# Kernel tuning notes

Hardware: AMD Instinct MI355X
Metric: run time of the kernel (lower is better)

## Reference

```python
import jax, jax.numpy as jnp
import numpy as np

N, NODE_DIM, EDGE_DIM, HID, NREL = 1024, 128, 32, 128, 16


def _sage(h, adj, W, b):
    # agg = mean over (weighted) neighbors: (adj @ h) / (deg + 1e-6)
    agg = (adj @ h) / (jnp.sum(adj, axis=1, keepdims=True) + 1e-6)
    return jax.nn.relu(jnp.concatenate([h, agg], axis=1) @ W.T + b)


def setup_inputs() -> dict:
    key = jax.random.key(0)
    ks = jax.random.split(key, 12)
    s1 = 1.0 / np.sqrt(2 * NODE_DIM)
    s2 = 1.0 / np.sqrt(2 * HID)
    s3 = 1.0 / np.sqrt(2 * HID + EDGE_DIM)
    s4 = 1.0 / np.sqrt(HID)
    return {
        "node_feat": jax.random.normal(ks[0], (N, NODE_DIM), jnp.float32),
        "edge_feat": jax.random.normal(ks[1], (N, N, EDGE_DIM), jnp.float32),
        "adj": jax.random.uniform(ks[2], (N, N), jnp.float32),
        "W_g1": jax.random.normal(ks[3], (HID, 2 * NODE_DIM), jnp.float32) * s1,
        "b_g1": jax.random.normal(ks[4], (HID,), jnp.float32) * s1,
        "W_g2": jax.random.normal(ks[5], (HID, 2 * HID), jnp.float32) * s2,
        "b_g2": jax.random.normal(ks[6], (HID,), jnp.float32) * s2,
        "W_c1": jax.random.normal(ks[7], (HID, 2 * HID + EDGE_DIM), jnp.float32) * s3,
        "b_c1": jax.random.normal(ks[8], (HID,), jnp.float32) * s3,
        "W_c2": jax.random.normal(ks[9], (NREL, HID), jnp.float32) * s4,
        "b_c2": jax.random.normal(ks[10], (NREL,), jnp.float32) * s4,
    }


def reference(node_feat, edge_feat, adj, W_g1, b_g1, W_g2, b_g2, W_c1, b_c1, W_c2, b_c2):
    h = _sage(node_feat, adj, W_g1, b_g1)          # [N, HID]
    h = _sage(h, adj, W_g2, b_g2)                  # [N, HID]
    H = h.shape[1]
    # Split first classifier layer over [h_i ; h_j ; e_ij] to avoid a huge concat.
    Wa, Wb, We = W_c1[:, :H], W_c1[:, H:2 * H], W_c1[:, 2 * H:]
    pre = ((h @ Wa.T)[:, None, :]
           + (h @ Wb.T)[None, :, :]
           + jnp.einsum('ije,he->ijh', edge_feat, We)
           + b_c1)                                  # [N, N, HID]
    logits = jax.nn.relu(pre) @ W_c2.T + b_c2       # [N, N, NREL]
    # diagonal (i == j) stays zero, matching the skipped loop iterations
    n = logits.shape[0]
    mask = 1.0 - jnp.eye(n, dtype=logits.dtype)
    return logits * mask[:, :, None]
```

## Files before the change

kernel.cpp:

```cpp
#include <hip/hip_runtime.h>
#include <hip/hip_bf16.h>
#include <stdint.h>

constexpr int NN = 1024;
constexpr int DD = 128;
constexpr int EDIM = 32;
constexpr int NR = 16;

using short4v = __attribute__((ext_vector_type(4))) short;
using short8v = __attribute__((ext_vector_type(8))) short;
using f32x4   = __attribute__((ext_vector_type(4))) float;

__device__ __forceinline__ short f2bf(float x) {
  __hip_bfloat16 h = __float2bfloat16(x);
  return __builtin_bit_cast(short, h);
}

__device__ __forceinline__ void nt_store4(float* p, const float4& v) {
  f32x4 t;
  t[0] = v.x; t[1] = v.y; t[2] = v.z; t[3] = v.w;
  __builtin_nontemporal_store(t, (f32x4*)p);
}

__global__ __launch_bounds__(256) void k_transp(const float* __restrict__ src,
                                                short* __restrict__ dst) {
  __shared__ float tile[32][33];
  int b = blockIdx.x;
  int r0 = (b & 31) * 32, c0 = (b >> 5) * 32;
  int t = threadIdx.x;
  {
    int rr = t >> 3, c4 = (t & 7) * 4;
    float4 v = *(const float4*)(src + (size_t)(r0 + rr) * DD + c0 + c4);
    tile[rr][c4]     = v.x;
    tile[rr][c4 + 1] = v.y;
    tile[rr][c4 + 2] = v.z;
    tile[rr][c4 + 3] = v.w;
  }
  __syncthreads();
  {
    int cc = t >> 3, r4 = (t & 7) * 4;
    short4v s;
    s[0] = f2bf(tile[r4 + 0][cc]);
    s[1] = f2bf(tile[r4 + 1][cc]);
    s[2] = f2bf(tile[r4 + 2][cc]);
    s[3] = f2bf(tile[r4 + 3][cc]);
    *(short4v*)(dst + (size_t)(c0 + cc) * NN + r0 + r4) = s;
  }
}

__global__ __launch_bounds__(256) void k_adjmm(const short* __restrict__ XT,
                                               const float* __restrict__ adj,
                                               float* __restrict__ part) {
  int t = threadIdx.x;
  int w = t >> 6, lane = t & 63;
  int c = lane & 15, g = lane >> 4;
  int b = blockIdx.x;
  int ic = b & 15, hc = (b >> 4) & 3, kc = b >> 6;
  int i0 = ic * 64 + w * 16, h0 = hc * 32;
  size_t kb = (size_t)kc * 256 + 8 * g;

  f32x4 acc0 = {0, 0, 0, 0}, acc1 = {0, 0, 0, 0};
  const short* xa0 = XT + (size_t)(h0 + c) * NN + kb;
  const short* xa1 = XT + (size_t)(h0 + 16 + c) * NN + kb;
  const float* ba  = adj + (size_t)(i0 + c) * NN + kb;
  #pragma unroll
  for (int ks = 0; ks < 8; ++ks) {
    short8v a0 = *(const short8v*)(xa0 + ks * 32);
    short8v a1 = *(const short8v*)(xa1 + ks * 32);
    float4 b0 = *(const float4*)(ba + ks * 32);
    float4 b1 = *(const float4*)(ba + ks * 32 + 4);
    short8v bb;
    bb[0] = f2bf(b0.x); bb[1] = f2bf(b0.y); bb[2] = f2bf(b0.z); bb[3] = f2bf(b0.w);
    bb[4] = f2bf(b1.x); bb[5] = f2bf(b1.y); bb[6] = f2bf(b1.z); bb[7] = f2bf(b1.w);
    acc0 = __builtin_amdgcn_mfma_f32_16x16x32_bf16(a0, bb, acc0, 0, 0, 0);
    acc1 = __builtin_amdgcn_mfma_f32_16x16x32_bf16(a1, bb, acc1, 0, 0, 0);
  }
  float* p0 = part + ((size_t)kc * NN + (i0 + c)) * DD + h0 + 4 * g;
  float4 o0 = {acc0[0], acc0[1], acc0[2], acc0[3]};
  float4 o1 = {acc1[0], acc1[1], acc1[2], acc1[3]};
  *(float4*)(p0)      = o0;
  *(float4*)(p0 + 16) = o1;
}

__global__ __launch_bounds__(256) void k_dense1(const float* __restrict__ X,
                                                const float* __restrict__ part,
                                                const float* __restrict__ adj,
                                                const float* __restrict__ W,
                                                const float* __restrict__ b,
                                                float* __restrict__ out,
                                                float* __restrict__ rsinv) {
  __shared__ float sagg[2][128];
  __shared__ float red[4];
  int t = threadIdx.x;
  int ig = t >> 7, h = t & 127;
  int i = blockIdx.x * 2 + ig;
  {
    const float4* ar = (const float4*)(adj + (size_t)i * NN);
    float4 v0 = ar[h * 2], v1 = ar[h * 2 + 1];
    float s = v0.x + v0.y + v0.z + v0.w + v1.x + v1.y + v1.z + v1.w;
    #pragma unroll
    for (int off = 32; off > 0; off >>= 1) s += __shfl_down(s, off, 64);
    if ((t & 63) == 0) red[t >> 6] = s;
  }
  __syncthreads();
  float rs = 1.0f / (red[ig * 2] + red[ig * 2 + 1] + 1e-6f);
  if (h == 0) rsinv[i] = rs;
  {
    float ss = 0.f;
    #pragma unroll
    for (int kc = 0; kc < 4; ++kc) ss += part[(size_t)kc * NN * DD + (size_t)i * DD + h];
    sagg[ig][h] = ss * rs;
  }
  __syncthreads();
  const float4* xr = (const float4*)(X + (size_t)i * DD);
  const float4* ar = (const float4*)(&sagg[ig][0]);
  const float4* w1 = (const float4*)(W + (size_t)h * 256);
  const float4* w2 = (const float4*)(W + (size_t)h * 256 + DD);
  float acc = b[h];
  #pragma unroll 8
  for (int k = 0; k < 32; ++k) {
    float4 x = xr[k], w = w1[k];
    acc += x.x * w.x + x.y * w.y + x.z * w.z + x.w * w.w;
  }
  #pragma unroll 8
  for (int k = 0; k < 32; ++k) {
    float4 y = ar[k], w = w2[k];
    acc += y.x * w.x + y.y * w.y + y.z * w.z + y.w * w.w;
  }
  out[(size_t)i * DD + h] = fmaxf(acc, 0.f);
}

__global__ __launch_bounds__(256) void k_dense2ab(const float* __restrict__ X,
                                                  const float* __restrict__ part,
                                                  const float* __restrict__ rsinv,
                                                  const float* __restrict__ W,
                                                  const float* __restrict__ b,
                                                  const float* __restrict__ Wc1,
                                                  const float* __restrict__ bc1,
                                                  float* __restrict__ Aib,
                                                  float* __restrict__ Bmat) {
  __shared__ float sagg[2][128];
  __shared__ float sh2[2][128];
  int t = threadIdx.x;
  int ig = t >> 7, h = t & 127;
  int i = blockIdx.x * 2 + ig;
  {
    float ss = 0.f;
    #pragma unroll
    for (int kc = 0; kc < 4; ++kc) ss += part[(size_t)kc * NN * DD + (size_t)i * DD + h];
    sagg[ig][h] = ss * rsinv[i];
  }
  __syncthreads();
  {
    const float4* xr = (const float4*)(X + (size_t)i * DD);
    const float4* ar = (const float4*)(&sagg[ig][0]);
    const float4* w1 = (const float4*)(W + (size_t)h * 256);
    const float4* w2 = (const float4*)(W + (size_t)h * 256 + DD);
    float acc = b[h];
    #pragma unroll 8
    for (int k = 0; k < 32; ++k) {
      float4 x = xr[k], w = w1[k];
      acc += x.x * w.x + x.y * w.y + x.z * w.z + x.w * w.w;
    }
    #pragma unroll 8
    for (int k = 0; k < 32; ++k) {
      float4 y = ar[k], w = w2[k];
      acc += y.x * w.x + y.y * w.y + y.z * w.z + y.w * w.w;
    }
    sh2[ig][h] = fmaxf(acc, 0.f);
  }
  __syncthreads();
  const float4* xr = (const float4*)(&sh2[ig][0]);
  const float4* wa = (const float4*)(Wc1 + (size_t)h * 288);
  const float4* wb = (const float4*)(Wc1 + (size_t)h * 288 + 128);
  float aa = bc1[h], bb = 0.f;
  #pragma unroll 8
  for (int k = 0; k < 32; ++k) {
    float4 x = xr[k];
    float4 a = wa[k], b2 = wb[k];
    aa += x.x * a.x + x.y * a.y + x.z * a.z + x.w * a.w;
    bb += x.x * b2.x + x.y * b2.y + x.z * b2.z + x.w * b2.w;
  }
  Aib[(size_t)i * DD + h] = aa;
  Bmat[(size_t)i * DD + h] = bb;
}

#define EDGE_BODY(T, S, PF) do {                                              \
    float4 a_ = eA##S, b_ = eB##S;                                            \
    if (PF) {                                                                 \
      const float* p_ = ebl + (size_t)((T) + 6) * ((size_t)NN * EDIM);        \
      eA##S = *(const float4*)p_;                                             \
      eB##S = *(const float4*)(p_ + 4);                                       \
    }                                                                         \
    short8v ef_;                                                              \
    ef_[0]=f2bf(a_.x); ef_[1]=f2bf(a_.y); ef_[2]=f2bf(a_.z); ef_[3]=f2bf(a_.w); \
    ef_[4]=f2bf(b_.x); ef_[5]=f2bf(b_.y); ef_[6]=f2bf(b_.z); ef_[7]=f2bf(b_.w); \
    char* pw_ = psm + (((T) & 1) << 12);                                      \
    const float* ap_ = aibs + (T) * 128 + 4 * g;                              \
    _Pragma("unroll")                                                         \
    for (int n = 0; n < 8; ++n) {                                             \
      float4 av_ = *(const float4*)(ap_ + 16 * n);                            \
      f32x4 ci_;                                                              \
      ci_[0] = av_.x + bjv[n].x; ci_[1] = av_.y + bjv[n].y;                   \
      ci_[2] = av_.z + bjv[n].z; ci_[3] = av_.w + bjv[n].w;                   \
      f32x4 acc_ = __builtin_amdgcn_mfma_f32_16x16x32_bf16(weF[n], ef_, ci_, 0, 0, 0); \
      short4v pk_;                                                            \
      pk_[0] = f2bf(fmaxf(acc_[0], 0.f)); pk_[1] = f2bf(fmaxf(acc_[1], 0.f)); \
      pk_[2] = f2bf(fmaxf(acc_[2], 0.f)); pk_[3] = f2bf(fmaxf(acc_[3], 0.f)); \
      *(short4v*)(pw_ + (((n >> 1) << 10) + ((n & 1) << 9) + wroff)) = pk_;   \
    }                                                                         \
  } while (0)

#define G2(G2T, OREG) do {                                                    \
    f32x4 a2_;                                                                \
    a2_[0] = bc2v.x; a2_[1] = bc2v.y; a2_[2] = bc2v.z; a2_[3] = bc2v.w;       \
    const char* pp_ = psm + (((G2T) & 1) << 12);                              \
    _Pragma("unroll")                                                         \
    for (int kk = 0; kk < 4; ++kk) {                                          \
      short8v pb_ = *(const short8v*)(pp_ + ((kk << 10) + rdP));              \
      a2_ = __builtin_amdgcn_mfma_f32_16x16x32_bf16(wcF[kk], pb_, a2_, 0, 0, 0); \
    }                                                                         \
    bool dg_ = (j == i0 + (G2T));                                             \
    OREG.x = dg_ ? 0.f : a2_[0];                                              \
    OREG.y = dg_ ? 0.f : a2_[1];                                              \
    OREG.z = dg_ ? 0.f : a2_[2];                                              \
    OREG.w = dg_ ? 0.f : a2_[3];                                              \
  } while (0)

#define FLUSH(BASE) do {                                                      \
    nt_store4(out + ((size_t)(i0 + (BASE) + 0) * NN + j) * NR + 4 * g, o0);   \
    nt_store4(out + ((size_t)(i0 + (BASE) + 1) * NN + j) * NR + 4 * g, o1);   \
    nt_store4(out + ((size_t)(i0 + (BASE) + 2) * NN + j) * NR + 4 * g, o2);   \
    nt_store4(out + ((size_t)(i0 + (BASE) + 3) * NN + j) * NR + 4 * g, o3);   \
  } while (0)

__global__ __launch_bounds__(256, 1) void k_edge(const float* __restrict__ edge,
                                                 const float* __restrict__ Wc1,
                                                 const float* __restrict__ Wc2,
                                                 const float* __restrict__ bc2,
                                                 const float* __restrict__ Aib,
                                                 const float* __restrict__ Bmat,
                                                 float* __restrict__ out) {
  __shared__ __align__(16) char psm_all[4][2][4096];
  __shared__ __align__(16) float aibs[16 * 128];
  int tid = threadIdx.x;
  int w = tid >> 6, lane = tid & 63;
  int c = lane & 15, g = lane >> 4;
  int ig = blockIdx.x >> 4, jg = blockIdx.x & 15;
  int i0 = ig * 16;
  int j0w = jg * 64 + w * 16;
  int j = j0w + c;

  {
    int ii = tid >> 4, h8 = (tid & 15) * 8;
    const float4* s = (const float4*)(Aib + (size_t)(i0 + ii) * DD + h8);
    *(float4*)(aibs + ii * 128 + h8)     = s[0];
    *(float4*)(aibs + ii * 128 + h8 + 4) = s[1];
  }

  short8v weF[8];
  #pragma unroll
  for (int n = 0; n < 8; ++n) {
    const float* p = Wc1 + (size_t)(16 * n + c) * 288 + 256 + 8 * g;
    float4 f0 = *(const float4*)p;
    float4 f1 = *(const float4*)(p + 4);
    short8v s;
    s[0]=f2bf(f0.x); s[1]=f2bf(f0.y); s[2]=f2bf(f0.z); s[3]=f2bf(f0.w);
    s[4]=f2bf(f1.x); s[5]=f2bf(f1.y); s[6]=f2bf(f1.z); s[7]=f2bf(f1.w);
    weF[n] = s;
  }
  short8v wcF[4];
  #pragma unroll
  for (int kk = 0; kk < 4; ++kk) {
    const float* p = Wc2 + (size_t)c * DD + 32 * kk + 8 * g;
    float4 f0 = *(const float4*)p;
    float4 f1 = *(const float4*)(p + 4);
    short8v s;
    s[0]=f2bf(f0.x); s[1]=f2bf(f0.y); s[2]=f2bf(f0.z); s[3]=f2bf(f0.w);
    s[4]=f2bf(f1.x); s[5]=f2bf(f1.y); s[6]=f2bf(f1.z); s[7]=f2bf(f1.w);
    wcF[kk] = s;
  }
  float4 bc2v = *(const float4*)(bc2 + 4 * g);
  float4 bjv[8];
  #pragma unroll
  for (int n = 0; n < 8; ++n)
    bjv[n] = *(const float4*)(Bmat + (size_t)j * DD + 16 * n + 4 * g);

  __syncthreads();

  char* psm = &psm_all[w][0][0];
  const float* ebl = edge + ((size_t)i0 * NN + j) * EDIM + 8 * g;
  int wroff = (c << 4) + ((g & 1) << 3) + ((g >> 1) << 8);
  int rdP   = (g << 8) + (c << 4);

  float4 o0, o1, o2, o3;

  float4 eA0, eB0, eA1, eB1, eA2, eB2, eA3, eB3, eA4, eB4, eA5, eB5;
  {
    const size_t STP = (size_t)NN * EDIM;
    eA0 = *(const float4*)(ebl);            eB0 = *(const float4*)(ebl + 4);
    eA1 = *(const float4*)(ebl + STP);      eB1 = *(const float4*)(ebl + STP + 4);
    eA2 = *(const float4*)(ebl + 2 * STP);  eB2 = *(const float4*)(ebl + 2 * STP + 4);
    eA3 = *(const float4*)(ebl + 3 * STP);  eB3 = *(const float4*)(ebl + 3 * STP + 4);
    eA4 = *(const float4*)(ebl + 4 * STP);  eB4 = *(const float4*)(ebl + 4 * STP + 4);
    eA5 = *(const float4*)(ebl + 5 * STP);  eB5 = *(const float4*)(ebl + 5 * STP + 4);
  }

  EDGE_BODY(0, 0, 1);
  EDGE_BODY(1, 1, 1);  G2(0, o0);
  EDGE_BODY(2, 2, 1);  G2(1, o1);
  EDGE_BODY(3, 3, 1);  G2(2, o2);
  EDGE_BODY(4, 4, 1);  G2(3, o3);  FLUSH(0);
  EDGE_BODY(5, 5, 1);  G2(4, o0);
  EDGE_BODY(6, 0, 1);  G2(5, o1);
  EDGE_BODY(7, 1, 1);  G2(6, o2);
  EDGE_BODY(8, 2, 1);  G2(7, o3);  FLUSH(4);
  EDGE_BODY(9, 3, 1);  G2(8, o0);
  EDGE_BODY(10, 4, 0); G2(9, o1);
  EDGE_BODY(11, 5, 0); G2(10, o2);
  EDGE_BODY(12, 0, 0); G2(11, o3); FLUSH(8);
  EDGE_BODY(13, 1, 0); G2(12, o0);
  EDGE_BODY(14, 2, 0); G2(13, o1);
  EDGE_BODY(15, 3, 0); G2(14, o2);
  G2(15, o3); FLUSH(12);
}

extern "C" void kernel_launch(void* const* d_in, const int* in_sizes, int n_in,
                              void* d_out, int out_size, void* d_ws, size_t ws_size,
                              hipStream_t stream) {
  const float* node_feat = (const float*)d_in[0];
  const float* edge_feat = (const float*)d_in[1];
  const float* adj  = (const float*)d_in[2];
  const float* W_g1 = (const float*)d_in[3];
  const float* b_g1 = (const float*)d_in[4];
  const float* W_g2 = (const float*)d_in[5];
  const float* b_g2 = (const float*)d_in[6];
  const float* W_c1 = (const float*)d_in[7];
  const float* b_c1 = (const float*)d_in[8];
  const float* W_c2 = (const float*)d_in[9];
  const float* b_c2 = (const float*)d_in[10];
  float* out = (float*)d_out;

  float* ws    = (float*)d_ws;
  float* rsinv = ws;
  float* part  = ws + 1024;
  float* h1    = part + 4 * NN * DD;
  float* Aib   = h1 + NN * DD;
  float* Bmat  = Aib + NN * DD;
  short* XT1   = (short*)(Bmat + NN * DD);
  short* XT2   = XT1 + DD * NN;

  k_transp<<<128, 256, 0, stream>>>(node_feat, XT1);
  k_adjmm<<<256, 256, 0, stream>>>(XT1, adj, part);
  k_dense1<<<512, 256, 0, stream>>>(node_feat, part, adj, W_g1, b_g1, h1, rsinv);
  k_transp<<<128, 256, 0, stream>>>(h1, XT2);
  k_adjmm<<<256, 256, 0, stream>>>(XT2, adj, part);
  k_dense2ab<<<512, 256, 0, stream>>>(h1, part, rsinv, W_g2, b_g2, W_c1, b_c1, Aib, Bmat);
  k_edge<<<1024, 256, 0, stream>>>(edge_feat, W_c1, W_c2, b_c2, Aib, Bmat, out);
}
```

Before: 122.8 us.

## Fuse transpose into adj matmul and cut edge-kernel registers for higher occupancy

```diff
diff --git a/kernel.cpp b/kernel.cpp
--- a/kernel.cpp
+++ b/kernel.cpp
@@ -16,53 +16,44 @@
   return __builtin_bit_cast(short, h);
 }
 
-__device__ __forceinline__ void nt_store4(float* p, const float4& v) {
-  f32x4 t;
-  t[0] = v.x; t[1] = v.y; t[2] = v.z; t[3] = v.w;
-  __builtin_nontemporal_store(t, (f32x4*)p);
-}
-
-__global__ __launch_bounds__(256) void k_transp(const float* __restrict__ src,
-                                                short* __restrict__ dst) {
-  __shared__ float tile[32][33];
-  int b = blockIdx.x;
-  int r0 = (b & 31) * 32, c0 = (b >> 5) * 32;
-  int t = threadIdx.x;
-  {
-    int rr = t >> 3, c4 = (t & 7) * 4;
-    float4 v = *(const float4*)(src + (size_t)(r0 + rr) * DD + c0 + c4);
-    tile[rr][c4]     = v.x;
-    tile[rr][c4 + 1] = v.y;
-    tile[rr][c4 + 2] = v.z;
-    tile[rr][c4 + 3] = v.w;
-  }
-  __syncthreads();
-  {
-    int cc = t >> 3, r4 = (t & 7) * 4;
-    short4v s;
-    s[0] = f2bf(tile[r4 + 0][cc]);
-    s[1] = f2bf(tile[r4 + 1][cc]);
-    s[2] = f2bf(tile[r4 + 2][cc]);
-    s[3] = f2bf(tile[r4 + 3][cc]);
-    *(short4v*)(dst + (size_t)(c0 + cc) * NN + r0 + r4) = s;
-  }
-}
-
-__global__ __launch_bounds__(256) void k_adjmm(const short* __restrict__ XT,
+__device__ __forceinline__ void nt_store4(float* p, const f32x4& v) {
+  __builtin_nontemporal_store(v, (f32x4*)p);
+}
+
+__global__ __launch_bounds__(256) void k_adjmm(const float* __restrict__ X,
                                                const float* __restrict__ adj,
                                                float* __restrict__ part) {
+  __shared__ short xt[32][264];
   int t = threadIdx.x;
   int w = t >> 6, lane = t & 63;
   int c = lane & 15, g = lane >> 4;
   int b = blockIdx.x;
   int ic = b & 15, hc = (b >> 4) & 3, kc = b >> 6;
   int i0 = ic * 64 + w * 16, h0 = hc * 32;
-  size_t kb = (size_t)kc * 256 + 8 * g;
+  int k0 = kc * 256;
+
+  {
+    const float* xr = X + (size_t)(k0 + t) * DD + h0;
+    #pragma unroll
+    for (int c8 = 0; c8 < 4; ++c8) {
+      float4 v0 = *(const float4*)(xr + c8 * 8);
+      float4 v1 = *(const float4*)(xr + c8 * 8 + 4);
+      xt[c8 * 8 + 0][t] = f2bf(v0.x);
+      xt[c8 * 8 + 1][t] = f2bf(v0.y);
+      xt[c8 * 8 + 2][t] = f2bf(v0.z);
+      xt[c8 * 8 + 3][t] = f2bf(v0.w);
+      xt[c8 * 8 + 4][t] = f2bf(v1.x);
+      xt[c8 * 8 + 5][t] = f2bf(v1.y);
+      xt[c8 * 8 + 6][t] = f2bf(v1.z);
+      xt[c8 * 8 + 7][t] = f2bf(v1.w);
+    }
+  }
+  __syncthreads();
 
   f32x4 acc0 = {0, 0, 0, 0}, acc1 = {0, 0, 0, 0};
-  const short* xa0 = XT + (size_t)(h0 + c) * NN + kb;
-  const short* xa1 = XT + (size_t)(h0 + 16 + c) * NN + kb;
-  const float* ba  = adj + (size_t)(i0 + c) * NN + kb;
+  const short* xa0 = &xt[c][8 * g];
+  const short* xa1 = &xt[16 + c][8 * g];
+  const float* ba  = adj + (size_t)(i0 + c) * NN + k0 + 8 * g;
   #pragma unroll
   for (int ks = 0; ks < 8; ++ks) {
     short8v a0 = *(const short8v*)(xa0 + ks * 32);
@@ -185,10 +176,11 @@
   Bmat[(size_t)i * DD + h] = bb;
 }
 
+
 #define EDGE_BODY(T, S, PF) do {                                              \
     float4 a_ = eA##S, b_ = eB##S;                                            \
     if (PF) {                                                                 \
-      const float* p_ = ebl + (size_t)((T) + 6) * ((size_t)NN * EDIM);        \
+      const float* p_ = ebl + (size_t)((T) + 4) * ((size_t)NN * EDIM);        \
       eA##S = *(const float4*)p_;                                             \
       eB##S = *(const float4*)(p_ + 4);                                       \
     }                                                                         \
@@ -200,9 +192,10 @@
     _Pragma("unroll")                                                         \
     for (int n = 0; n < 8; ++n) {                                             \
       float4 av_ = *(const float4*)(ap_ + 16 * n);                            \
+      float4 bv_ = *(const float4*)(bp + 16 * n);           \
       f32x4 ci_;                                                              \
-      ci_[0] = av_.x + bjv[n].x; ci_[1] = av_.y + bjv[n].y;                   \
-      ci_[2] = av_.z + bjv[n].z; ci_[3] = av_.w + bjv[n].w;                   \
+      ci_[0] = av_.x + bv_.x; ci_[1] = av_.y + bv_.y;                         \
+      ci_[2] = av_.z + bv_.z; ci_[3] = av_.w + bv_.w;                         \
       f32x4 acc_ = __builtin_amdgcn_mfma_f32_16x16x32_bf16(weF[n], ef_, ci_, 0, 0, 0); \
       short4v pk_;                                                            \
       pk_[0] = f2bf(fmaxf(acc_[0], 0.f)); pk_[1] = f2bf(fmaxf(acc_[1], 0.f)); \
@@ -211,7 +204,7 @@
     }                                                                         \
   } while (0)
 
-#define G2(G2T, OREG) do {                                                    \
+#define G2_ST(G2T) do {                                                       \
     f32x4 a2_;                                                                \
     a2_[0] = bc2v.x; a2_[1] = bc2v.y; a2_[2] = bc2v.z; a2_[3] = bc2v.w;       \
     const char* pp_ = psm + (((G2T) & 1) << 12);                              \
@@ -221,20 +214,15 @@
       a2_ = __builtin_amdgcn_mfma_f32_16x16x32_bf16(wcF[kk], pb_, a2_, 0, 0, 0); \
     }                                                                         \
     bool dg_ = (j == i0 + (G2T));                                             \
-    OREG.x = dg_ ? 0.f : a2_[0];                                              \
-    OREG.y = dg_ ? 0.f : a2_[1];                                              \
-    OREG.z = dg_ ? 0.f : a2_[2];                                              \
-    OREG.w = dg_ ? 0.f : a2_[3];                                              \
+    f32x4 o_;                                                                 \
+    o_[0] = dg_ ? 0.f : a2_[0];                                               \
+    o_[1] = dg_ ? 0.f : a2_[1];                                               \
+    o_[2] = dg_ ? 0.f : a2_[2];                                               \
+    o_[3] = dg_ ? 0.f : a2_[3];                                               \
+    nt_store4(out + ((size_t)(i0 + (G2T)) * NN + j) * NR + 4 * g, o_);        \
   } while (0)
 
-#define FLUSH(BASE) do {                                                      \
-    nt_store4(out + ((size_t)(i0 + (BASE) + 0) * NN + j) * NR + 4 * g, o0);   \
-    nt_store4(out + ((size_t)(i0 + (BASE) + 1) * NN + j) * NR + 4 * g, o1);   \
-    nt_store4(out + ((size_t)(i0 + (BASE) + 2) * NN + j) * NR + 4 * g, o2);   \
-    nt_store4(out + ((size_t)(i0 + (BASE) + 3) * NN + j) * NR + 4 * g, o3);   \
-  } while (0)
-
-__global__ __launch_bounds__(256, 1) void k_edge(const float* __restrict__ edge,
+__global__ __launch_bounds__(256, 3) void k_edge(const float* __restrict__ edge,
                                                  const float* __restrict__ Wc1,
                                                  const float* __restrict__ Wc2,
                                                  const float* __restrict__ bc2,
@@ -281,10 +269,7 @@
     wcF[kk] = s;
   }
   float4 bc2v = *(const float4*)(bc2 + 4 * g);
-  float4 bjv[8];
-  #pragma unroll
-  for (int n = 0; n < 8; ++n)
-    bjv[n] = *(const float4*)(Bmat + (size_t)j * DD + 16 * n + 4 * g);
+  const float* bp = Bmat + (size_t)j * DD + 4 * g;
 
   __syncthreads();
 
@@ -293,36 +278,32 @@
   int wroff = (c << 4) + ((g & 1) << 3) + ((g >> 1) << 8);
   int rdP   = (g << 8) + (c << 4);
 
-  float4 o0, o1, o2, o3;
-
-  float4 eA0, eB0, eA1, eB1, eA2, eB2, eA3, eB3, eA4, eB4, eA5, eB5;
+  float4 eA0, eB0, eA1, eB1, eA2, eB2, eA3, eB3;
   {
     const size_t STP = (size_t)NN * EDIM;
     eA0 = *(const float4*)(ebl);            eB0 = *(const float4*)(ebl + 4);
     eA1 = *(const float4*)(ebl + STP);      eB1 = *(const float4*)(ebl + STP + 4);
     eA2 = *(const float4*)(ebl + 2 * STP);  eB2 = *(const float4*)(ebl + 2 * STP + 4);
     eA3 = *(const float4*)(ebl + 3 * STP);  eB3 = *(const float4*)(ebl + 3 * STP + 4);
-    eA4 = *(const float4*)(ebl + 4 * STP);  eB4 = *(const float4*)(ebl + 4 * STP + 4);
-    eA5 = *(const float4*)(ebl + 5 * STP);  eB5 = *(const float4*)(ebl + 5 * STP + 4);
-  }
-
-  EDGE_BODY(0, 0, 1);
-  EDGE_BODY(1, 1, 1);  G2(0, o0);
-  EDGE_BODY(2, 2, 1);  G2(1, o1);
-  EDGE_BODY(3, 3, 1);  G2(2, o2);
-  EDGE_BODY(4, 4, 1);  G2(3, o3);  FLUSH(0);
-  EDGE_BODY(5, 5, 1);  G2(4, o0);
-  EDGE_BODY(6, 0, 1);  G2(5, o1);
-  EDGE_BODY(7, 1, 1);  G2(6, o2);
-  EDGE_BODY(8, 2, 1);  G2(7, o3);  FLUSH(4);
-  EDGE_BODY(9, 3, 1);  G2(8, o0);
-  EDGE_BODY(10, 4, 0); G2(9, o1);
-  EDGE_BODY(11, 5, 0); G2(10, o2);
-  EDGE_BODY(12, 0, 0); G2(11, o3); FLUSH(8);
-  EDGE_BODY(13, 1, 0); G2(12, o0);
-  EDGE_BODY(14, 2, 0); G2(13, o1);
-  EDGE_BODY(15, 3, 0); G2(14, o2);
-  G2(15, o3); FLUSH(12);
+  }
+
+  EDGE_BODY(0,  0, 1);
+  EDGE_BODY(1,  1, 1);  G2_ST(0);
+  EDGE_BODY(2,  2, 1);  G2_ST(1);
+  EDGE_BODY(3,  3, 1);  G2_ST(2);
+  EDGE_BODY(4,  0, 1);  G2_ST(3);
+  EDGE_BODY(5,  1, 1);  G2_ST(4);
+  EDGE_BODY(6,  2, 1);  G2_ST(5);
+  EDGE_BODY(7,  3, 1);  G2_ST(6);
+  EDGE_BODY(8,  0, 1);  G2_ST(7);
+  EDGE_BODY(9,  1, 1);  G2_ST(8);
+  EDGE_BODY(10, 2, 1);  G2_ST(9);
+  EDGE_BODY(11, 3, 1);  G2_ST(10);
+  EDGE_BODY(12, 0, 0);  G2_ST(11);
+  EDGE_BODY(13, 1, 0);  G2_ST(12);
+  EDGE_BODY(14, 2, 0);  G2_ST(13);
+  EDGE_BODY(15, 3, 0);  G2_ST(14);
+  G2_ST(15);
 }
 
 extern "C" void kernel_launch(void* const* d_in, const int* in_sizes, int n_in,
@@ -347,14 +328,10 @@
   float* h1    = part + 4 * NN * DD;
   float* Aib   = h1 + NN * DD;
   float* Bmat  = Aib + NN * DD;
-  short* XT1   = (short*)(Bmat + NN * DD);
-  short* XT2   = XT1 + DD * NN;
-
-  k_transp<<<128, 256, 0, stream>>>(node_feat, XT1);
-  k_adjmm<<<256, 256, 0, stream>>>(XT1, adj, part);
+
+  k_adjmm<<<256, 256, 0, stream>>>(node_feat, adj, part);
   k_dense1<<<512, 256, 0, stream>>>(node_feat, part, adj, W_g1, b_g1, h1, rsinv);
-  k_transp<<<128, 256, 0, stream>>>(h1, XT2);
-  k_adjmm<<<256, 256, 0, stream>>>(XT2, adj, part);
+  k_adjmm<<<256, 256, 0, stream>>>(h1, adj, part);
   k_dense2ab<<<512, 256, 0, stream>>>(h1, part, rsinv, W_g2, b_g2, W_c1, b_c1, Aib, Bmat);
   k_edge<<<1024, 256, 0, stream>>>(edge_feat, W_c1, W_c2, b_c2, Aib, Bmat, out);
 }
```

Measured after the change: 236.4 us. 1.93x slower.
